# Kernel tuning notes

Measured on AMD Instinct MI355X. Metric: run time of the kernel, lower is better.

## Reference

```python
import jax, jax.numpy as jnp
import numpy as np

N_NODES = 50000
N_EDGES = 1600000
IN_FEATS = 128
ENC_H = 20
DEC_H = 64


def setup_inputs() -> dict:
    key = jax.random.key(0)
    ks = jax.random.split(key, 14)
    inp = {}
    inp["x"] = jax.random.normal(ks[0], (N_NODES, IN_FEATS), dtype=jnp.float32)
    inp["edge_index"] = jax.random.randint(ks[1], (2, N_EDGES), 0, N_NODES, dtype=jnp.int64)
    inp["node_id"] = 0
    inp["noise_normal"] = jax.random.normal(ks[2], (N_EDGES, ENC_H), dtype=jnp.float32)
    inp["noise_u"] = jax.random.uniform(ks[3], (N_EDGES, 1), dtype=jnp.float32)
    # parameters (glorot-ish init)
    def lin(k, fan_in, fan_out):
        s = 1.0 / np.sqrt(fan_in)
        return jax.random.uniform(k, (fan_in, fan_out), jnp.float32, -s, s)
    inp["W_gc"] = lin(ks[4], IN_FEATS, ENC_H)
    inp["b_gc"] = jnp.zeros((ENC_H,), jnp.float32)
    inp["W_mu"] = lin(ks[5], 3 * ENC_H, ENC_H)
    inp["b_mu"] = jnp.zeros((ENC_H,), jnp.float32)
    inp["W_var"] = lin(ks[6], 3 * ENC_H, ENC_H)
    inp["b_var"] = jnp.zeros((ENC_H,), jnp.float32)
    inp["W_d1"] = lin(ks[7], ENC_H, DEC_H)
    inp["b_d1"] = jnp.zeros((DEC_H,), jnp.float32)
    inp["W_d2"] = lin(ks[8], DEC_H, 1)
    inp["b_d2"] = jnp.zeros((1,), jnp.float32)
    return inp


def _gcn_conv(x, edge_index, W, b):
    """PyG-style GCNConv: add self-loops, symmetric D^-1/2 (A+I) D^-1/2 norm."""
    n = x.shape[0]
    sl = jnp.arange(n, dtype=edge_index.dtype)
    row = jnp.concatenate([edge_index[0], sl])  # source
    col = jnp.concatenate([edge_index[1], sl])  # target
    xw = x @ W  # [N, H]
    deg = jax.ops.segment_sum(jnp.ones_like(col, dtype=xw.dtype), col, num_segments=n)
    dinv = jnp.where(deg > 0, jax.lax.rsqrt(deg), 0.0)
    norm = dinv[row] * dinv[col]  # [E+N]
    out = jax.ops.segment_sum(xw[row] * norm[:, None], col, num_segments=n)
    return out + b


def reference(x, edge_index, node_id, noise_normal, noise_u,
              W_gc, b_gc, W_mu, b_mu, W_var, b_var, W_d1, b_d1, W_d2, b_d2):
    # GCN encoder
    x1 = jax.nn.relu(_gcn_conv(x, edge_index, W_gc, b_gc))  # [N, H]
    # per-edge concat: [src_embed | dst_embed | node_id_embed]
    rows, cols = edge_index[0], edge_index[1]
    node_embed = jnp.broadcast_to(x1[node_id][None, :], (rows.shape[0], x1.shape[1]))
    x2 = jnp.concatenate([x1[rows], x1[cols], node_embed], axis=1)  # [E, 3H]
    # variational heads + reparameterization
    mu = x2 @ W_mu + b_mu
    sigma = jnp.exp(x2 @ W_var + b_var)
    z = mu + sigma * noise_normal  # [E, H]
    # decoder MLP
    h = jax.nn.relu(z @ W_d1 + b_d1)
    sampling_weights = jax.nn.relu(h @ W_d2 + b_d2)  # [E, 1]
    # gumbel-sigmoid sample (training=True, bias=0.0 -> bias'=1e-4, temperature=1.0)
    bias = 0.0001
    eps = (bias - (1.0 - bias)) * noise_u + (1.0 - bias)
    gate = jnp.log(eps) - jnp.log(1.0 - eps) + sampling_weights
    return jax.nn.sigmoid(gate)
```

## Files before the change

### kernel.cpp

```cpp
#include <hip/hip_runtime.h>

#define NFEAT 128
#define H 20
#define DH 64
#define SCAN_T 1024
#define BE 64
#define NB 192
#define HW 12800

typedef __attribute__((ext_vector_type(8))) short short8;
typedef __attribute__((ext_vector_type(4))) float f32x4;

__device__ __forceinline__ unsigned short f2bf(float f) {
    union { float f; unsigned u; } v; v.f = f;
    unsigned r = v.u + 0x7fff + ((v.u >> 16) & 1);
    return (unsigned short)(r >> 16);
}
__device__ __forceinline__ unsigned pk2(unsigned short a, unsigned short b) {
    return (unsigned)a | ((unsigned)b << 16);
}

template <int CTRL>
__device__ __forceinline__ float dpp_add(float x) {
    int y = __builtin_amdgcn_update_dpp(0, __float_as_int(x), CTRL, 0xF, 0xF, true);
    return x + __int_as_float(y);
}
__device__ __forceinline__ float sum16(float x) {
    x = dpp_add<0xB1>(x);
    x = dpp_add<0x4E>(x);
    x = dpp_add<0x124>(x);
    x = dpp_add<0x128>(x);
    return x;
}

__global__ __launch_bounds__(256) void k_prep(const float* __restrict__ Wmu, const float* __restrict__ Wvar,
                                              const float* __restrict__ Wd1,
                                              unsigned short* __restrict__ Bh, unsigned short* __restrict__ Bd1,
                                              int* __restrict__ deg, int* __restrict__ csum, int N) {
    int t = blockIdx.x * blockDim.x + threadIdx.x;
    if (t < N) deg[t] = 0;
    if (t < 256) csum[t] = 0;
    if (t < 512) {
        int f = t >> 6, l = t & 63;
        int tile = f >> 1, s = f & 1;
        int col = (tile & 1) * 16 + (l & 15);
        const float* W = (tile < 2) ? Wmu : Wvar;
#pragma unroll
        for (int j = 0; j < 8; j++) {
            int k = s * 32 + (l >> 4) * 8 + j;
            float v = (k < 2 * H && col < H) ? W[k * H + col] : 0.f;
            Bh[(size_t)f * 512 + l * 8 + j] = f2bf(v);
        }
    } else if (t < 768) {
        int f = (t - 512) >> 6, l = t & 63;
        int n = f * 16 + (l & 15);
#pragma unroll
        for (int j = 0; j < 8; j++) {
            int k = (l >> 4) * 8 + j;
            float v = (k < H) ? Wd1[k * DH + n] : 0.f;
            Bd1[(size_t)f * 512 + l * 8 + j] = f2bf(v);
        }
    }
}

__global__ __launch_bounds__(512) void k_hist(const int* __restrict__ cols,
                                              unsigned* __restrict__ hist, int* __restrict__ csum,
                                              int E, int N) {
    __shared__ unsigned h[HW];
    __shared__ int cs[256];
    int wstride = (N + 3) >> 2;
    int nchunks = (N + 255) >> 8;
    for (int i = threadIdx.x; i < wstride; i += 512) h[i] = 0;
    if (threadIdx.x < 256) cs[threadIdx.x] = 0;
    __syncthreads();
    int chunk = (E + NB - 1) / NB;
    int beg = blockIdx.x * chunk, end = min(beg + chunk, E);
    for (int i = beg + threadIdx.x; i < end; i += 512) {
        int c = __builtin_nontemporal_load(cols + i);
        atomicAdd(&h[c >> 2], 1u << ((c & 3) * 8));
    }
    __syncthreads();
    unsigned* dst = hist + (size_t)blockIdx.x * wstride;
    for (int i = threadIdx.x; i < wstride; i += 512) {
        unsigned w = h[i];
        dst[i] = w;
        if (w) {
            int s = (w & 0xFF) + ((w >> 8) & 0xFF) + ((w >> 16) & 0xFF) + (w >> 24);
            atomicAdd(&cs[i >> 6], s);
        }
    }
    __syncthreads();
    for (int j = threadIdx.x; j < nchunks; j += 512)
        if (cs[j]) atomicAdd(&csum[j], cs[j]);
}

__global__ __launch_bounds__(256) void k_scansmall(const int* __restrict__ chunkSum,
                                                   int* __restrict__ chunkOff, int nb) {
    __shared__ int sc[256];
    int t = threadIdx.x;
    int v0 = (t < nb) ? chunkSum[t] : 0;
    sc[t] = v0;
    __syncthreads();
    for (int off = 1; off < 256; off <<= 1) {
        int v = (t >= off) ? sc[t - off] : 0;
        __syncthreads();
        sc[t] += v;
        __syncthreads();
    }
    if (t < nb) chunkOff[t] = sc[t] - v0;
}

__global__ __launch_bounds__(256) void k_bases(const unsigned* __restrict__ hist,
                                               const int* __restrict__ chunkOff,
                                               unsigned char* __restrict__ delta,
                                               int* __restrict__ offsets, int* __restrict__ deg,
                                               int N, int E) {
    __shared__ int sc[256];
    int c = blockIdx.x * 256 + threadIdx.x;
    int wstride = (N + 3) >> 2;
    int sh = (c & 3) * 8;
    bool valid = c < N;
    int cw = valid ? (c >> 2) : 0;
    unsigned cnt[NB / 4];
    int d = 0;
#pragma unroll
    for (int b = 0; b < NB; b++) {
        unsigned w = hist[(size_t)b * wstride + cw];
        unsigned byte = (w >> sh) & 0xFF;
        if ((b & 3) == 0) cnt[b >> 2] = byte;
        else cnt[b >> 2] |= byte << ((b & 3) * 8);
        d += (int)byte;
    }
    if (!valid) d = 0;
    sc[threadIdx.x] = d;
    __syncthreads();
    for (int off = 1; off < 256; off <<= 1) {
        int v = (threadIdx.x >= off) ? sc[threadIdx.x - off] : 0;
        __syncthreads();
        sc[threadIdx.x] += v;
        __syncthreads();
    }
    if (valid) {
        int base = chunkOff[blockIdx.x] + sc[threadIdx.x] - d;
        offsets[c] = base;
        deg[c] = d;
        int run = 0;
#pragma unroll
        for (int b = 0; b < NB; b++) {
            delta[(size_t)b * N + c] = (unsigned char)run;
            run += (int)((cnt[b >> 2] >> ((b & 3) * 8)) & 0xFF);
        }
    }
    if (blockIdx.x == 0 && threadIdx.x == 0) offsets[N] = E;
}

__global__ __launch_bounds__(512) void k_place(const int* __restrict__ rows, const int* __restrict__ cols,
                                               const int* __restrict__ offsets,
                                               const unsigned char* __restrict__ delta,
                                               unsigned short* __restrict__ srcs, int E, int N) {
    __shared__ unsigned h[HW];
    int wstride = (N + 3) >> 2;
    for (int i = threadIdx.x; i < wstride; i += 512) h[i] = 0;
    __syncthreads();
    int chunk = (E + NB - 1) / NB;
    int beg = blockIdx.x * chunk, end = min(beg + chunk, E);
    const unsigned char* mydelta = delta + (size_t)blockIdx.x * N;
    for (int i = beg + threadIdx.x; i < end; i += 512) {
        int c = __builtin_nontemporal_load(cols + i);
        int r = __builtin_nontemporal_load(rows + i);
        int sh = (c & 3) * 8;
        unsigned old = atomicAdd(&h[c >> 2], 1u << sh);
        int rank = (old >> sh) & 0xFF;
        int pos = offsets[c] + (int)mydelta[c] + rank;
        srcs[pos] = (unsigned short)r;
    }
}

__global__ __launch_bounds__(256) void k_deg(const int* __restrict__ cols, int* __restrict__ deg, int E) {
    int t = blockIdx.x * blockDim.x + threadIdx.x;
    if (t < E) atomicAdd(&deg[cols[t]], 1);
}

__global__ __launch_bounds__(SCAN_T) void k_scan(const int* __restrict__ deg, int* __restrict__ offsets,
                                                 int* __restrict__ cursor, int N) {
    __shared__ int sums[SCAN_T];
    int t = threadIdx.x;
    int chunk = (N + SCAN_T - 1) / SCAN_T;
    int beg = t * chunk;
    int end = min(beg + chunk, N);
    int s = 0;
    for (int i = beg; i < end; i++) s += deg[i];
    sums[t] = s;
    __syncthreads();
    for (int off = 1; off < SCAN_T; off <<= 1) {
        int v = (t >= off) ? sums[t - off] : 0;
        __syncthreads();
        sums[t] += v;
        __syncthreads();
    }
    int run = (t == 0) ? 0 : sums[t - 1];
    for (int i = beg; i < end; i++) {
        offsets[i] = run;
        cursor[i] = run;
        run += deg[i];
    }
    if (t == SCAN_T - 1) offsets[N] = sums[SCAN_T - 1];
}

__global__ __launch_bounds__(256) void k_bucket_csr(const int* __restrict__ rows, const int* __restrict__ cols,
                                                    int* __restrict__ cursor, int* __restrict__ srcs, int E) {
    int e = blockIdx.x * blockDim.x + threadIdx.x;
    if (e >= E) return;
    int pos = atomicAdd(&cursor[cols[e]], 1);
    srcs[pos] = rows[e];
}

__global__ __launch_bounds__(256) void k_xw_xs(const float* __restrict__ x, const float* __restrict__ Wgc,
                                               const int* __restrict__ deg,
                                               float* __restrict__ xs, int N) {
    __shared__ float Ws[NFEAT * H];
    for (int i = threadIdx.x; i < NFEAT * H; i += blockDim.x) Ws[i] = Wgc[i];
    __syncthreads();
    int n = blockIdx.x * blockDim.x + threadIdx.x;
    if (n >= N) return;
    float acc[H];
#pragma unroll
    for (int j = 0; j < H; j++) acc[j] = 0.f;
    const float4* x4 = (const float4*)(x + (size_t)n * NFEAT);
#pragma unroll 4
    for (int k4 = 0; k4 < NFEAT / 4; k4++) {
        float4 xv = x4[k4];
#pragma unroll
        for (int s = 0; s < 4; s++) {
            float xk = (s == 0) ? xv.x : (s == 1) ? xv.y : (s == 2) ? xv.z : xv.w;
            const float4* wrow = (const float4*)(Ws + (k4 * 4 + s) * H);
#pragma unroll
            for (int q = 0; q < 5; q++) {
                float4 w = wrow[q];
                acc[q * 4 + 0] += xk * w.x;
                acc[q * 4 + 1] += xk * w.y;
                acc[q * 4 + 2] += xk * w.z;
                acc[q * 4 + 3] += xk * w.w;
            }
        }
    }
    float di = rsqrtf((float)(deg[n] + 1));
    float4* o = (float4*)(xs + (size_t)n * H);
#pragma unroll
    for (int q = 0; q < 5; q++)
        o[q] = make_float4(acc[q * 4 + 0] * di, acc[q * 4 + 1] * di, acc[q * 4 + 2] * di, acc[q * 4 + 3] * di);
}

template <typename IT>
__device__ __forceinline__ void gather_core16(const float* __restrict__ xs, const IT* __restrict__ idx,
                                              int beg, int end, int n, int sl, int degn,
                                              const float* __restrict__ bgc, unsigned short* __restrict__ x1b,
                                              int nid, const float* __restrict__ Wmu, const float* __restrict__ Wvar,
                                              const float* __restrict__ bmu, const float* __restrict__ bvar,
                                              float* __restrict__ bcat2) {
    float acc[H];
    if (sl == 0) {
        const float4* self = (const float4*)(xs + (size_t)n * H);
#pragma unroll
        for (int q = 0; q < 5; q++) {
            float4 v = self[q];
            acc[q * 4 + 0] = v.x; acc[q * 4 + 1] = v.y; acc[q * 4 + 2] = v.z; acc[q * 4 + 3] = v.w;
        }
    } else {
#pragma unroll
        for (int j = 0; j < H; j++) acc[j] = 0.f;
    }
#pragma unroll 2
    for (int i = beg + sl; i < end; i += 16) {
        int r = (int)__builtin_nontemporal_load(idx + i);
        const float4* p = (const float4*)(xs + (size_t)r * H);
#pragma unroll
        for (int q = 0; q < 5; q++) {
            float4 v = p[q];
            acc[q * 4 + 0] += v.x; acc[q * 4 + 1] += v.y; acc[q * 4 + 2] += v.z; acc[q * 4 + 3] += v.w;
        }
    }
#pragma unroll
    for (int j = 0; j < H; j++) acc[j] = sum16(acc[j]);
    float di = rsqrtf((float)(degn + 1));
    float x1f[H];
#pragma unroll
    for (int j = 0; j < H; j++) x1f[j] = fmaxf(di * acc[j] + bgc[j], 0.f);
    if (sl == 0) {
        unsigned o[10];
#pragma unroll
        for (int j = 0; j < 10; j++) o[j] = pk2(f2bf(x1f[2 * j]), f2bf(x1f[2 * j + 1]));
        unsigned* dst = (unsigned*)(x1b + (size_t)n * H);
        *(uint4*)dst = make_uint4(o[0], o[1], o[2], o[3]);
        *(uint4*)(dst + 4) = make_uint4(o[4], o[5], o[6], o[7]);
        *(uint2*)(dst + 8) = make_uint2(o[8], o[9]);
    }
    if (n == nid) {
#pragma unroll
        for (int base = 0; base < 48; base += 16) {
            int jj = base + sl;
            if (jj < 40) {
                bool ismu = jj < 20;
                int col = ismu ? jj : jj - 20;
                const float* W = ismu ? Wmu : Wvar;
                float s = ismu ? bmu[col] : bvar[col];
#pragma unroll
                for (int k = 0; k < H; k++) s += x1f[k] * W[(2 * H + k) * H + col];
                bcat2[jj] = s;
            }
        }
    }
}

__global__ __launch_bounds__(256) void k_gather_csr16(const float* __restrict__ xs, const unsigned short* __restrict__ srcs,
                                                      const int* __restrict__ offsets, const int* __restrict__ deg,
                                                      const float* __restrict__ bgc,
                                                      unsigned short* __restrict__ x1b,
                                                      const int* __restrict__ node_id,
                                                      const float* __restrict__ Wmu, const float* __restrict__ Wvar,
                                                      const float* __restrict__ bmu, const float* __restrict__ bvar,
                                                      float* __restrict__ bcat2, int N) {
    int wave = (blockIdx.x * 256 + threadIdx.x) >> 6;
    int lane = threadIdx.x & 63;
    int n = wave * 4 + (lane >> 4);
    if (n >= N) return;
    gather_core16(xs, srcs, offsets[n], offsets[n + 1], n, lane & 15, deg[n], bgc, x1b,
                  node_id[0], Wmu, Wvar, bmu, bvar, bcat2);
}

__global__ __launch_bounds__(256) void k_gather_csr(const float* __restrict__ xs, const int* __restrict__ srcs,
                                                    const int* __restrict__ offsets, const int* __restrict__ deg,
                                                    const float* __restrict__ bgc,
                                                    unsigned short* __restrict__ x1b,
                                                    const int* __restrict__ node_id,
                                                    const float* __restrict__ Wmu, const float* __restrict__ Wvar,
                                                    const float* __restrict__ bmu, const float* __restrict__ bvar,
                                                    float* __restrict__ bcat2, int N) {
    int wave = (blockIdx.x * 256 + threadIdx.x) >> 6;
    int lane = threadIdx.x & 63;
    int n = wave * 4 + (lane >> 4);
    if (n >= N) return;
    gather_core16(xs, srcs, offsets[n], offsets[n + 1], n, lane & 15, deg[n], bgc, x1b,
                  node_id[0], Wmu, Wvar, bmu, bvar, bcat2);
}

__global__ __launch_bounds__(256, 8) void k_mlp(
    const unsigned short* __restrict__ x1b, const int* __restrict__ rows, const int* __restrict__ cols,
    const float* __restrict__ noise_n, const float* __restrict__ noise_u,
    const unsigned short* __restrict__ Bh, const unsigned short* __restrict__ Bd1g,
    const float* __restrict__ bcat2, const float* __restrict__ b_d1,
    const float* __restrict__ W_d2, const float* __restrict__ b_d2,
    float* __restrict__ out, int E) {

    __shared__ __align__(16) unsigned short x2s[BE * 72];
    __shared__ __align__(16) unsigned short A2[BE * 44];

    int tid = threadIdx.x;
    int e0 = blockIdx.x * BE;
    int l = tid & 63, w = tid >> 6;
    int m = l & 15, quad = l >> 4;
    int erow0 = w * 16 + quad * 4;

    float nz0[4], nz1[4];
#pragma unroll
    for (int r4 = 0; r4 < 4; r4++) {
        int e = e0 + erow0 + r4;
        int ec = (e < E) ? e : 0;
        nz0[r4] = noise_n[(size_t)ec * H + m];
        nz1[r4] = (m < 4) ? noise_n[(size_t)ec * H + 16 + m] : 0.f;
    }

    {
        int le = tid >> 2, p = tid & 3;
        int e = e0 + le; if (e >= E) e = E - 1;
        int r = rows[e], c = cols[e];
#pragma unroll
        for (int ii = 0; ii < 4; ii++) {
            int i = p + ii * 4;
            unsigned* dst = (unsigned*)((char*)x2s + le * 144 + i * 8);
            if (i < 10) {
                int node = (i < 5) ? r : c;
                int cc = (i < 5) ? i : i - 5;
                uint2 v = *(const uint2*)((const char*)x1b + (size_t)node * 40 + cc * 8);
                dst[0] = v.x;
                dst[1] = v.y;
            } else {
                dst[0] = 0u; dst[1] = 0u;
            }
        }
    }
    __syncthreads();

    f32x4 accs[4];
    {
        const char* arow = (const char*)x2s + (w * 16 + m) * 144 + quad * 16;
        short8 a0 = *(const short8*)(arow);
        short8 a1 = *(const short8*)(arow + 64);
#pragma unroll
        for (int t4 = 0; t4 < 4; t4++) {
            f32x4 acc = {0.f, 0.f, 0.f, 0.f};
            short8 b0 = *(const short8*)(Bh + (t4 * 2 + 0) * 512 + l * 8);
            short8 b1 = *(const short8*)(Bh + (t4 * 2 + 1) * 512 + l * 8);
            acc = __builtin_amdgcn_mfma_f32_16x16x32_bf16(a0, b0, acc, 0, 0, 0);
            acc = __builtin_amdgcn_mfma_f32_16x16x32_bf16(a1, b1, acc, 0, 0, 0);
            accs[t4] = acc;
        }
    }

    {
        float bm0 = bcat2[m];
        float bv0 = bcat2[20 + m];
        float bm1 = (m < 4) ? bcat2[16 + m] : 0.f;
        float bv1 = (m < 4) ? bcat2[36 + m] : 0.f;
#pragma unroll
        for (int r4 = 0; r4 < 4; r4++) {
            float z0 = accs[0][r4] + bm0 + __expf(accs[2][r4] + bv0) * nz0[r4];
            *(unsigned short*)((char*)A2 + (erow0 + r4) * 88 + m * 2) = f2bf(z0);
            unsigned short z1v = 0;
            if (m < 4) z1v = f2bf(accs[1][r4] + bm1 + __expf(accs[3][r4] + bv1) * nz1[r4]);
            *(unsigned short*)((char*)A2 + (erow0 + r4) * 88 + (16 + m) * 2) = z1v;
        }
    }
    __syncthreads();

    {
        short8 a2 = *(const short8*)((const char*)A2 + (w * 16 + m) * 88 + quad * 16);
        float p0 = 0.f, p1 = 0.f, p2 = 0.f, p3 = 0.f;
#pragma unroll
        for (int t4 = 0; t4 < 4; t4++) {
            f32x4 acc = {0.f, 0.f, 0.f, 0.f};
            short8 bb = *(const short8*)(Bd1g + t4 * 512 + l * 8);
            acc = __builtin_amdgcn_mfma_f32_16x16x32_bf16(a2, bb, acc, 0, 0, 0);
            int col = t4 * 16 + m;
            float bias = b_d1[col], wo = W_d2[col];
            p0 += fmaxf(acc[0] + bias, 0.f) * wo;
            p1 += fmaxf(acc[1] + bias, 0.f) * wo;
            p2 += fmaxf(acc[2] + bias, 0.f) * wo;
            p3 += fmaxf(acc[3] + bias, 0.f) * wo;
        }
        p0 = sum16(p0); p1 = sum16(p1); p2 = sum16(p2); p3 = sum16(p3);
        if (m < 4) {
            float swv = (m == 0) ? p0 : (m == 1) ? p1 : (m == 2) ? p2 : p3;
            int leo = w * 16 + quad * 4 + m;
            int e = e0 + leo;
            if (e < E) {
                float sw = fmaxf(swv + b_d2[0], 0.f);
                float u = noise_u[e];
                float ev = 0.9999f - 0.9998f * u;
                float t = __expf(-sw);
                out[e] = ev / (ev + (1.f - ev) * t);
            }
        }
    }
}

extern "C" void kernel_launch(void* const* d_in, const int* in_sizes, int n_in,
                              void* d_out, int out_size, void* d_ws, size_t ws_size,
                              hipStream_t stream) {
    const int N = in_sizes[0] / NFEAT;
    const int E = in_sizes[1] / 2;

    const float* x       = (const float*)d_in[0];
    const int*   ei      = (const int*)d_in[1];
    const int*   rows    = ei;
    const int*   cols    = ei + E;
    const int*   node_id = (const int*)d_in[2];
    const float* noise_n = (const float*)d_in[3];
    const float* noise_u = (const float*)d_in[4];
    const float* Wgc  = (const float*)d_in[5];
    const float* bgc  = (const float*)d_in[6];
    const float* Wmu  = (const float*)d_in[7];
    const float* bmu  = (const float*)d_in[8];
    const float* Wvar = (const float*)d_in[9];
    const float* bvar = (const float*)d_in[10];
    const float* Wd1  = (const float*)d_in[11];
    const float* bd1  = (const float*)d_in[12];
    const float* Wd2  = (const float*)d_in[13];
    const float* bd2  = (const float*)d_in[14];
    float* out = (float*)d_out;

    const int B = 256;
    int gN  = (N + B - 1) / B;
    int gG  = (N + 15) / 16;
    int gE  = (E + B - 1) / B;
    int gM  = (E + BE - 1) / BE;
    int nBins = (N + 255) / 256;

    char* ws = (char*)d_ws;
    size_t o_deg     = 0;
    size_t o_off     = o_deg  + (((size_t)N * 4 + 255) & ~255ULL);
    size_t o_csum    = o_off  + (((size_t)(N + 1) * 4 + 255) & ~255ULL);
    size_t o_coff    = o_csum + 1024;
    size_t o_hist    = o_coff + 1024;
    size_t wstride   = (size_t)((N + 3) >> 2);
    size_t o_delta   = o_hist  + ((NB * wstride * 4 + 255) & ~255ULL);
    size_t o_srcs    = o_delta + (((size_t)NB * N + 255) & ~255ULL);
    size_t o_xs      = o_srcs  + (((size_t)E * 2 + 255) & ~255ULL);
    size_t o_x1b     = o_xs    + (((size_t)N * H * 4 + 255) & ~255ULL);
    size_t o_Bh      = o_x1b   + (((size_t)N * H * 2 + 255) & ~255ULL);
    size_t o_Bd1     = o_Bh    + 8192;
    size_t o_bcat2   = o_Bd1   + 4096;
    size_t need      = o_bcat2 + 256;

    bool main_path = (ws_size >= need) && (N <= 4 * HW) && (N < 65536) && (nBins <= 256);

    if (main_path) {
        int*   deg     = (int*)(ws + o_deg);
        int*   offsets = (int*)(ws + o_off);
        int*   csum    = (int*)(ws + o_csum);
        int*   coff    = (int*)(ws + o_coff);
        unsigned* hist = (unsigned*)(ws + o_hist);
        unsigned char* delta = (unsigned char*)(ws + o_delta);
        unsigned short* srcs = (unsigned short*)(ws + o_srcs);
        float* xs      = (float*)(ws + o_xs);
        unsigned short* x1b  = (unsigned short*)(ws + o_x1b);
        unsigned short* Bh   = (unsigned short*)(ws + o_Bh);
        unsigned short* Bd1  = (unsigned short*)(ws + o_Bd1);
        float* bcat2   = (float*)(ws + o_bcat2);

        k_prep<<<gN, B, 0, stream>>>(Wmu, Wvar, Wd1, Bh, Bd1, deg, csum, N);
        k_hist<<<NB, 512, 0, stream>>>(cols, hist, csum, E, N);
        k_scansmall<<<1, B, 0, stream>>>(csum, coff, nBins);
        k_bases<<<nBins, B, 0, stream>>>(hist, coff, delta, offsets, deg, N, E);
        k_xw_xs<<<gN, B, 0, stream>>>(x, Wgc, deg, xs, N);
        k_place<<<NB, 512, 0, stream>>>(rows, cols, offsets, delta, srcs, E, N);
        k_gather_csr16<<<gG, B, 0, stream>>>(xs, srcs, offsets, deg, bgc, x1b,
                                             node_id, Wmu, Wvar, bmu, bvar, bcat2, N);
        k_mlp<<<gM, B, 0, stream>>>(x1b, rows, cols, noise_n, noise_u,
                                    Bh, Bd1, bcat2, bd1, Wd2, bd2, out, E);
    } else {
        int*   deg     = (int*)ws;
        int*   offsets = (int*)(ws + 200000);
        int*   cursor  = (int*)(ws + 400016);
        int*   srcs    = (int*)(ws + 600016);
        float* xs      = (float*)(ws + 7000016);
        unsigned short* x1b = (unsigned short*)(ws + 11000016);
        unsigned short* Bh  = (unsigned short*)(ws + 13000016);
        unsigned short* Bd1 = (unsigned short*)(ws + 13008208);
        float* bcat2   = (float*)(ws + 13012304);

        k_prep<<<gN, B, 0, stream>>>(Wmu, Wvar, Wd1, Bh, Bd1, deg, cursor, N);
        k_deg<<<gE, B, 0, stream>>>(cols, deg, E);
        k_scan<<<1, SCAN_T, 0, stream>>>(deg, offsets, cursor, N);
        k_bucket_csr<<<gE, B, 0, stream>>>(rows, cols, cursor, srcs, E);
        k_xw_xs<<<gN, B, 0, stream>>>(x, Wgc, deg, xs, N);
        k_gather_csr<<<gG, B, 0, stream>>>(xs, srcs, offsets, deg, bgc, x1b,
                                           node_id, Wmu, Wvar, bmu, bvar, bcat2, N);
        k_mlp<<<gM, B, 0, stream>>>(x1b, rows, cols, noise_n, noise_u,
                                    Bh, Bd1, bcat2, bd1, Wd2, bd2, out, E);
    }
}
```

Before: 430.4 us.

## Record per-edge rank in histogram pass and drop LDS from edge MLP

The histogram kernel now saves each edge's within-block rank from its shared-memory atomic into a byte array. The placement kernel therefore becomes a simple per-edge scatter with no shared histogram rebuild. The edge MLP kernel is restructured to compute the transposed product: each lane loads its edge's embeddings straight from global memory as the MFMA operand, and the intermediate z is shuffled with ds_bpermute instead of two LDS round-trips and barriers. This adds an E-byte rank buffer and extra writes, and changes the bcat2 layout, which is now zero-initialised in prep.

```diff
diff --git a/kernel.cpp b/kernel.cpp
--- a/kernel.cpp
+++ b/kernel.cpp
@@ -35,21 +35,23 @@
 
 __global__ __launch_bounds__(256) void k_prep(const float* __restrict__ Wmu, const float* __restrict__ Wvar,
                                               const float* __restrict__ Wd1,
-                                              unsigned short* __restrict__ Bh, unsigned short* __restrict__ Bd1,
-                                              int* __restrict__ deg, int* __restrict__ csum, int N) {
+                                              unsigned short* __restrict__ Bh2, unsigned short* __restrict__ Bd1,
+                                              int* __restrict__ deg, int* __restrict__ csum,
+                                              float* __restrict__ bcat2, int N) {
     int t = blockIdx.x * blockDim.x + threadIdx.x;
     if (t < N) deg[t] = 0;
     if (t < 256) csum[t] = 0;
+    if (t < 128) bcat2[t] = 0.f;
     if (t < 512) {
         int f = t >> 6, l = t & 63;
-        int tile = f >> 1, s = f & 1;
-        int col = (tile & 1) * 16 + (l & 15);
-        const float* W = (tile < 2) ? Wmu : Wvar;
+        int h = f >> 2, tt = (f >> 1) & 1, s = f & 1;
+        const float* W = h ? Wvar : Wmu;
+        int d = tt * 16 + (l & 15);
 #pragma unroll
         for (int j = 0; j < 8; j++) {
             int k = s * 32 + (l >> 4) * 8 + j;
-            float v = (k < 2 * H && col < H) ? W[k * H + col] : 0.f;
-            Bh[(size_t)f * 512 + l * 8 + j] = f2bf(v);
+            float v = (k < 2 * H && d < H) ? W[k * H + d] : 0.f;
+            Bh2[(size_t)f * 512 + l * 8 + j] = f2bf(v);
         }
     } else if (t < 768) {
         int f = (t - 512) >> 6, l = t & 63;
@@ -65,6 +67,7 @@
 
 __global__ __launch_bounds__(512) void k_hist(const int* __restrict__ cols,
                                               unsigned* __restrict__ hist, int* __restrict__ csum,
+                                              unsigned char* __restrict__ rank,
                                               int E, int N) {
     __shared__ unsigned h[HW];
     __shared__ int cs[256];
@@ -77,7 +80,9 @@
     int beg = blockIdx.x * chunk, end = min(beg + chunk, E);
     for (int i = beg + threadIdx.x; i < end; i += 512) {
         int c = __builtin_nontemporal_load(cols + i);
-        atomicAdd(&h[c >> 2], 1u << ((c & 3) * 8));
+        int sh = (c & 3) * 8;
+        unsigned old = atomicAdd(&h[c >> 2], 1u << sh);
+        rank[i] = (unsigned char)((old >> sh) & 0xFF);
     }
     __syncthreads();
     unsigned* dst = hist + (size_t)blockIdx.x * wstride;
@@ -154,26 +159,18 @@
     if (blockIdx.x == 0 && threadIdx.x == 0) offsets[N] = E;
 }
 
-__global__ __launch_bounds__(512) void k_place(const int* __restrict__ rows, const int* __restrict__ cols,
+__global__ __launch_bounds__(256) void k_place(const int* __restrict__ rows, const int* __restrict__ cols,
                                                const int* __restrict__ offsets,
                                                const unsigned char* __restrict__ delta,
-                                               unsigned short* __restrict__ srcs, int E, int N) {
-    __shared__ unsigned h[HW];
-    int wstride = (N + 3) >> 2;
-    for (int i = threadIdx.x; i < wstride; i += 512) h[i] = 0;
-    __syncthreads();
-    int chunk = (E + NB - 1) / NB;
-    int beg = blockIdx.x * chunk, end = min(beg + chunk, E);
-    const unsigned char* mydelta = delta + (size_t)blockIdx.x * N;
-    for (int i = beg + threadIdx.x; i < end; i += 512) {
-        int c = __builtin_nontemporal_load(cols + i);
-        int r = __builtin_nontemporal_load(rows + i);
-        int sh = (c & 3) * 8;
-        unsigned old = atomicAdd(&h[c >> 2], 1u << sh);
-        int rank = (old >> sh) & 0xFF;
-        int pos = offsets[c] + (int)mydelta[c] + rank;
-        srcs[pos] = (unsigned short)r;
-    }
+                                               const unsigned char* __restrict__ rank,
+                                               unsigned short* __restrict__ srcs, int E, int N, int chunk) {
+    int e = blockIdx.x * 256 + threadIdx.x;
+    if (e >= E) return;
+    int c = cols[e];
+    int r = rows[e];
+    int b = e / chunk;
+    int pos = offsets[c] + (int)delta[(size_t)b * N + c] + (int)rank[e];
+    srcs[pos] = (unsigned short)r;
 }
 
 __global__ __launch_bounds__(256) void k_deg(const int* __restrict__ cols, int* __restrict__ deg, int E) {
@@ -306,7 +303,7 @@
                 float s = ismu ? bmu[col] : bvar[col];
 #pragma unroll
                 for (int k = 0; k < H; k++) s += x1f[k] * W[(2 * H + k) * H + col];
-                bcat2[jj] = s;
+                bcat2[ismu ? col : 64 + col] = s;
             }
         }
     }
@@ -344,112 +341,123 @@
                   node_id[0], Wmu, Wvar, bmu, bvar, bcat2);
 }
 
-__global__ __launch_bounds__(256, 8) void k_mlp(
+__global__ __launch_bounds__(256) void k_mlp(
     const unsigned short* __restrict__ x1b, const int* __restrict__ rows, const int* __restrict__ cols,
     const float* __restrict__ noise_n, const float* __restrict__ noise_u,
-    const unsigned short* __restrict__ Bh, const unsigned short* __restrict__ Bd1g,
+    const unsigned short* __restrict__ Bh2, const unsigned short* __restrict__ Bd1g,
     const float* __restrict__ bcat2, const float* __restrict__ b_d1,
     const float* __restrict__ W_d2, const float* __restrict__ b_d2,
     float* __restrict__ out, int E) {
 
-    __shared__ __align__(16) unsigned short x2s[BE * 72];
-    __shared__ __align__(16) unsigned short A2[BE * 44];
-
     int tid = threadIdx.x;
     int e0 = blockIdx.x * BE;
     int l = tid & 63, w = tid >> 6;
-    int m = l & 15, quad = l >> 4;
-    int erow0 = w * 16 + quad * 4;
-
-    float nz0[4], nz1[4];
-#pragma unroll
-    for (int r4 = 0; r4 < 4; r4++) {
-        int e = e0 + erow0 + r4;
-        int ec = (e < E) ? e : 0;
-        nz0[r4] = noise_n[(size_t)ec * H + m];
-        nz1[r4] = (m < 4) ? noise_n[(size_t)ec * H + 16 + m] : 0.f;
-    }
-
-    {
-        int le = tid >> 2, p = tid & 3;
-        int e = e0 + le; if (e >= E) e = E - 1;
-        int r = rows[e], c = cols[e];
-#pragma unroll
-        for (int ii = 0; ii < 4; ii++) {
-            int i = p + ii * 4;
-            unsigned* dst = (unsigned*)((char*)x2s + le * 144 + i * 8);
-            if (i < 10) {
-                int node = (i < 5) ? r : c;
-                int cc = (i < 5) ? i : i - 5;
-                uint2 v = *(const uint2*)((const char*)x1b + (size_t)node * 40 + cc * 8);
-                dst[0] = v.x;
-                dst[1] = v.y;
-            } else {
-                dst[0] = 0u; dst[1] = 0u;
-            }
-        }
-    }
-    __syncthreads();
+    int m = l & 15, g = l >> 4;
+
+    int ea = e0 + w * 16 + m;
+    int em = (ea < E) ? ea : E - 1;
+    int r = rows[em], c = cols[em];
+
+    const char* br = (const char*)x1b + (size_t)r * 40;
+    const char* bc = (const char*)x1b + (size_t)c * 40;
+    const char* a0p = (g == 0) ? br : (g == 1) ? br + 16 : (g == 2) ? br + 32 : bc + 8;
+    const char* a1p = (g == 0) ? br + 8 : (g == 1) ? br + 24 : (g == 2) ? bc : bc + 16;
+    uint2 f0a = *(const uint2*)a0p;
+    uint2 f0b = *(const uint2*)a1p;
+    union U8 { unsigned u[4]; short8 s; };
+    U8 B0u, B1u;
+    B0u.u[0] = f0a.x; B0u.u[1] = f0a.y; B0u.u[2] = f0b.x; B0u.u[3] = f0b.y;
+    B1u.u[0] = 0u; B1u.u[1] = 0u; B1u.u[2] = 0u; B1u.u[3] = 0u;
+    if (g == 0) {
+        uint2 f1a = *(const uint2*)(bc + 24);
+        uint2 f1b = *(const uint2*)(bc + 32);
+        B1u.u[0] = f1a.x; B1u.u[1] = f1a.y; B1u.u[2] = f1b.x; B1u.u[3] = f1b.y;
+    }
+
+    float4 nz0 = *(const float4*)(noise_n + (size_t)em * H + g * 4);
+    float4 bm0 = *(const float4*)(bcat2 + g * 4);
+    float4 bv0 = *(const float4*)(bcat2 + 64 + g * 4);
+    float4 nz1 = make_float4(0.f, 0.f, 0.f, 0.f), bm1 = nz1, bv1 = nz1;
+    if (g == 0) {
+        nz1 = *(const float4*)(noise_n + (size_t)em * H + 16);
+        bm1 = *(const float4*)(bcat2 + 16);
+        bv1 = *(const float4*)(bcat2 + 80);
+    }
 
     f32x4 accs[4];
-    {
-        const char* arow = (const char*)x2s + (w * 16 + m) * 144 + quad * 16;
-        short8 a0 = *(const short8*)(arow);
-        short8 a1 = *(const short8*)(arow + 64);
-#pragma unroll
-        for (int t4 = 0; t4 < 4; t4++) {
-            f32x4 acc = {0.f, 0.f, 0.f, 0.f};
-            short8 b0 = *(const short8*)(Bh + (t4 * 2 + 0) * 512 + l * 8);
-            short8 b1 = *(const short8*)(Bh + (t4 * 2 + 1) * 512 + l * 8);
-            acc = __builtin_amdgcn_mfma_f32_16x16x32_bf16(a0, b0, acc, 0, 0, 0);
-            acc = __builtin_amdgcn_mfma_f32_16x16x32_bf16(a1, b1, acc, 0, 0, 0);
-            accs[t4] = acc;
-        }
-    }
-
-    {
-        float bm0 = bcat2[m];
-        float bv0 = bcat2[20 + m];
-        float bm1 = (m < 4) ? bcat2[16 + m] : 0.f;
-        float bv1 = (m < 4) ? bcat2[36 + m] : 0.f;
-#pragma unroll
-        for (int r4 = 0; r4 < 4; r4++) {
-            float z0 = accs[0][r4] + bm0 + __expf(accs[2][r4] + bv0) * nz0[r4];
-            *(unsigned short*)((char*)A2 + (erow0 + r4) * 88 + m * 2) = f2bf(z0);
-            unsigned short z1v = 0;
-            if (m < 4) z1v = f2bf(accs[1][r4] + bm1 + __expf(accs[3][r4] + bv1) * nz1[r4]);
-            *(unsigned short*)((char*)A2 + (erow0 + r4) * 88 + (16 + m) * 2) = z1v;
-        }
-    }
-    __syncthreads();
-
-    {
-        short8 a2 = *(const short8*)((const char*)A2 + (w * 16 + m) * 88 + quad * 16);
-        float p0 = 0.f, p1 = 0.f, p2 = 0.f, p3 = 0.f;
-#pragma unroll
-        for (int t4 = 0; t4 < 4; t4++) {
-            f32x4 acc = {0.f, 0.f, 0.f, 0.f};
-            short8 bb = *(const short8*)(Bd1g + t4 * 512 + l * 8);
-            acc = __builtin_amdgcn_mfma_f32_16x16x32_bf16(a2, bb, acc, 0, 0, 0);
-            int col = t4 * 16 + m;
-            float bias = b_d1[col], wo = W_d2[col];
-            p0 += fmaxf(acc[0] + bias, 0.f) * wo;
-            p1 += fmaxf(acc[1] + bias, 0.f) * wo;
-            p2 += fmaxf(acc[2] + bias, 0.f) * wo;
-            p3 += fmaxf(acc[3] + bias, 0.f) * wo;
-        }
-        p0 = sum16(p0); p1 = sum16(p1); p2 = sum16(p2); p3 = sum16(p3);
-        if (m < 4) {
-            float swv = (m == 0) ? p0 : (m == 1) ? p1 : (m == 2) ? p2 : p3;
-            int leo = w * 16 + quad * 4 + m;
-            int e = e0 + leo;
-            if (e < E) {
-                float sw = fmaxf(swv + b_d2[0], 0.f);
-                float u = noise_u[e];
-                float ev = 0.9999f - 0.9998f * u;
-                float t = __expf(-sw);
-                out[e] = ev / (ev + (1.f - ev) * t);
-            }
+#pragma unroll
+    for (int q4 = 0; q4 < 4; q4++) {
+        f32x4 acc = {0.f, 0.f, 0.f, 0.f};
+        short8 A0 = *(const short8*)(Bh2 + (q4 * 2 + 0) * 512 + l * 8);
+        short8 A1 = *(const short8*)(Bh2 + (q4 * 2 + 1) * 512 + l * 8);
+        acc = __builtin_amdgcn_mfma_f32_16x16x32_bf16(A0, B0u.s, acc, 0, 0, 0);
+        acc = __builtin_amdgcn_mfma_f32_16x16x32_bf16(A1, B1u.s, acc, 0, 0, 0);
+        accs[q4] = acc;
+    }
+
+    float nza[4] = {nz0.x, nz0.y, nz0.z, nz0.w};
+    float bma[4] = {bm0.x, bm0.y, bm0.z, bm0.w};
+    float bva[4] = {bv0.x, bv0.y, bv0.z, bv0.w};
+    float nzb[4] = {nz1.x, nz1.y, nz1.z, nz1.w};
+    float bmb[4] = {bm1.x, bm1.y, bm1.z, bm1.w};
+    float bvb[4] = {bv1.x, bv1.y, bv1.z, bv1.w};
+    float z0[4], z1[4];
+#pragma unroll
+    for (int rr = 0; rr < 4; rr++) {
+        z0[rr] = accs[0][rr] + bma[rr] + __expf(accs[2][rr] + bva[rr]) * nza[rr];
+        z1[rr] = 0.f;
+    }
+    if (g == 0) {
+#pragma unroll
+        for (int rr = 0; rr < 4; rr++)
+            z1[rr] = accs[1][rr] + bmb[rr] + __expf(accs[3][rr] + bvb[rr]) * nzb[rr];
+    }
+    unsigned pz0 = pk2(f2bf(z0[0]), f2bf(z0[1]));
+    unsigned pz1 = pk2(f2bf(z0[2]), f2bf(z0[3]));
+    unsigned pz2 = pk2(f2bf(z1[0]), f2bf(z1[1]));
+    unsigned pz3 = pk2(f2bf(z1[2]), f2bf(z1[3]));
+
+    int sA = (((2 * g) & 3) * 16 + m) * 4;
+    int sB = (((2 * g + 1) & 3) * 16 + m) * 4;
+    unsigned qA0 = (unsigned)__builtin_amdgcn_ds_bpermute(sA, (int)pz0);
+    unsigned qA1 = (unsigned)__builtin_amdgcn_ds_bpermute(sA, (int)pz1);
+    unsigned qB0 = (unsigned)__builtin_amdgcn_ds_bpermute(sB, (int)pz0);
+    unsigned qB1 = (unsigned)__builtin_amdgcn_ds_bpermute(sB, (int)pz1);
+    unsigned qA2 = (unsigned)__builtin_amdgcn_ds_bpermute(sA, (int)pz2);
+    unsigned qA3 = (unsigned)__builtin_amdgcn_ds_bpermute(sA, (int)pz3);
+    unsigned qB2 = (unsigned)__builtin_amdgcn_ds_bpermute(sB, (int)pz2);
+    unsigned qB3 = (unsigned)__builtin_amdgcn_ds_bpermute(sB, (int)pz3);
+    bool hi = (g == 2);
+    U8 A2u;
+    A2u.u[0] = (g == 3) ? 0u : (hi ? qA2 : qA0);
+    A2u.u[1] = (g == 3) ? 0u : (hi ? qA3 : qA1);
+    A2u.u[2] = (g == 3) ? 0u : (hi ? qB2 : qB0);
+    A2u.u[3] = (g == 3) ? 0u : (hi ? qB3 : qB1);
+    short8 a2 = A2u.s;
+
+    float p0 = 0.f, p1 = 0.f, p2 = 0.f, p3 = 0.f;
+#pragma unroll
+    for (int t4 = 0; t4 < 4; t4++) {
+        f32x4 acc = {0.f, 0.f, 0.f, 0.f};
+        short8 bb = *(const short8*)(Bd1g + t4 * 512 + l * 8);
+        acc = __builtin_amdgcn_mfma_f32_16x16x32_bf16(a2, bb, acc, 0, 0, 0);
+        int col = t4 * 16 + m;
+        float bias = b_d1[col], wo = W_d2[col];
+        p0 += fmaxf(acc[0] + bias, 0.f) * wo;
+        p1 += fmaxf(acc[1] + bias, 0.f) * wo;
+        p2 += fmaxf(acc[2] + bias, 0.f) * wo;
+        p3 += fmaxf(acc[3] + bias, 0.f) * wo;
+    }
+    p0 = sum16(p0); p1 = sum16(p1); p2 = sum16(p2); p3 = sum16(p3);
+    if (m < 4) {
+        float swv = (m == 0) ? p0 : (m == 1) ? p1 : (m == 2) ? p2 : p3;
+        int e = e0 + w * 16 + g * 4 + m;
+        if (e < E) {
+            float sw = fmaxf(swv + b_d2[0], 0.f);
+            float u = noise_u[e];
+            float ev = 0.9999f - 0.9998f * u;
+            float t = __expf(-sw);
+            out[e] = ev / (ev + (1.f - ev) * t);
         }
     }
 }
@@ -485,22 +493,24 @@
     int gE  = (E + B - 1) / B;
     int gM  = (E + BE - 1) / BE;
     int nBins = (N + 255) / 256;
+    int chunk = (E + NB - 1) / NB;
 
     char* ws = (char*)d_ws;
+    size_t wstride   = (size_t)((N + 3) >> 2);
     size_t o_deg     = 0;
     size_t o_off     = o_deg  + (((size_t)N * 4 + 255) & ~255ULL);
     size_t o_csum    = o_off  + (((size_t)(N + 1) * 4 + 255) & ~255ULL);
     size_t o_coff    = o_csum + 1024;
     size_t o_hist    = o_coff + 1024;
-    size_t wstride   = (size_t)((N + 3) >> 2);
     size_t o_delta   = o_hist  + ((NB * wstride * 4 + 255) & ~255ULL);
-    size_t o_srcs    = o_delta + (((size_t)NB * N + 255) & ~255ULL);
+    size_t o_rank    = o_delta + (((size_t)NB * N + 255) & ~255ULL);
+    size_t o_srcs    = o_rank  + (((size_t)E + 255) & ~255ULL);
     size_t o_xs      = o_srcs  + (((size_t)E * 2 + 255) & ~255ULL);
     size_t o_x1b     = o_xs    + (((size_t)N * H * 4 + 255) & ~255ULL);
-    size_t o_Bh      = o_x1b   + (((size_t)N * H * 2 + 255) & ~255ULL);
-    size_t o_Bd1     = o_Bh    + 8192;
+    size_t o_Bh2     = o_x1b   + (((size_t)N * H * 2 + 255) & ~255ULL);
+    size_t o_Bd1     = o_Bh2   + 8192;
     size_t o_bcat2   = o_Bd1   + 4096;
-    size_t need      = o_bcat2 + 256;
+    size_t need      = o_bcat2 + 512;
 
     bool main_path = (ws_size >= need) && (N <= 4 * HW) && (N < 65536) && (nBins <= 256);
 
@@ -511,35 +521,46 @@
         int*   coff    = (int*)(ws + o_coff);
         unsigned* hist = (unsigned*)(ws + o_hist);
         unsigned char* delta = (unsigned char*)(ws + o_delta);
+        unsigned char* rank  = (unsigned char*)(ws + o_rank);
         unsigned short* srcs = (unsigned short*)(ws + o_srcs);
         float* xs      = (float*)(ws + o_xs);
         unsigned short* x1b  = (unsigned short*)(ws + o_x1b);
-        unsigned short* Bh   = (unsigned short*)(ws + o_Bh);
+        unsigned short* Bh2  = (unsigned short*)(ws + o_Bh2);
         unsigned short* Bd1  = (unsigned short*)(ws + o_Bd1);
         float* bcat2   = (float*)(ws + o_bcat2);
 
-        k_prep<<<gN, B, 0, stream>>>(Wmu, Wvar, Wd1, Bh, Bd1, deg, csum, N);
-        k_hist<<<NB, 512, 0, stream>>>(cols, hist, csum, E, N);
+        k_prep<<<gN, B, 0, stream>>>(Wmu, Wvar, Wd1, Bh2, Bd1, deg, csum, bcat2, N);
+        k_hist<<<NB, 512, 0, stream>>>(cols, hist, csum, rank, E, N);
         k_scansmall<<<1, B, 0, stream>>>(csum, coff, nBins);
         k_bases<<<nBins, B, 0, stream>>>(hist, coff, delta, offsets, deg, N, E);
         k_xw_xs<<<gN, B, 0, stream>>>(x, Wgc, deg, xs, N);
-        k_place<<<NB, 512, 0, stream>>>(rows, cols, offsets, delta, srcs, E, N);
+        k_place<<<gE, B, 0, stream>>>(rows, cols, offsets, delta, rank, srcs, E, N, chunk);
         k_gather_csr16<<<gG, B, 0, stream>>>(xs, srcs, offsets, deg, bgc, x1b,
                                              node_id, Wmu, Wvar, bmu, bvar, bcat2, N);
         k_mlp<<<gM, B, 0, stream>>>(x1b, rows, cols, noise_n, noise_u,
-                                    Bh, Bd1, bcat2, bd1, Wd2, bd2, out, E);
+                                    Bh2, Bd1, bcat2, bd1, Wd2, bd2, out, E);
     } else {
-        int*   deg     = (int*)ws;
-        int*   offsets = (int*)(ws + 200000);
-        int*   cursor  = (int*)(ws + 400016);
-        int*   srcs    = (int*)(ws + 600016);
-        float* xs      = (float*)(ws + 7000016);
-        unsigned short* x1b = (unsigned short*)(ws + 11000016);
-        unsigned short* Bh  = (unsigned short*)(ws + 13000016);
-        unsigned short* Bd1 = (unsigned short*)(ws + 13008208);
-        float* bcat2   = (float*)(ws + 13012304);
-
-        k_prep<<<gN, B, 0, stream>>>(Wmu, Wvar, Wd1, Bh, Bd1, deg, cursor, N);
+        size_t f_deg   = 0;
+        size_t f_off   = f_deg + (((size_t)N * 4 + 255) & ~255ULL);
+        size_t f_cur   = f_off + (((size_t)(N + 1) * 4 + 255) & ~255ULL);
+        size_t f_srcs  = f_cur + (((size_t)N * 4 + 255) & ~255ULL);
+        size_t f_xs    = f_srcs + (((size_t)E * 4 + 255) & ~255ULL);
+        size_t f_x1b   = f_xs + (((size_t)N * H * 4 + 255) & ~255ULL);
+        size_t f_Bh2   = f_x1b + (((size_t)N * H * 2 + 255) & ~255ULL);
+        size_t f_Bd1   = f_Bh2 + 8192;
+        size_t f_bcat2 = f_Bd1 + 4096;
+
+        int*   deg     = (int*)(ws + f_deg);
+        int*   offsets = (int*)(ws + f_off);
+        int*   cursor  = (int*)(ws + f_cur);
+        int*   srcs    = (int*)(ws + f_srcs);
+        float* xs      = (float*)(ws + f_xs);
+        unsigned short* x1b = (unsigned short*)(ws + f_x1b);
+        unsigned short* Bh2 = (unsigned short*)(ws + f_Bh2);
+        unsigned short* Bd1 = (unsigned short*)(ws + f_Bd1);
+        float* bcat2   = (float*)(ws + f_bcat2);
+
+        k_prep<<<gN, B, 0, stream>>>(Wmu, Wvar, Wd1, Bh2, Bd1, deg, cursor, bcat2, N);
         k_deg<<<gE, B, 0, stream>>>(cols, deg, E);
         k_scan<<<1, SCAN_T, 0, stream>>>(deg, offsets, cursor, N);
         k_bucket_csr<<<gE, B, 0, stream>>>(rows, cols, cursor, srcs, E);
@@ -547,6 +568,6 @@
         k_gather_csr<<<gG, B, 0, stream>>>(xs, srcs, offsets, deg, bgc, x1b,
                                            node_id, Wmu, Wvar, bmu, bvar, bcat2, N);
         k_mlp<<<gM, B, 0, stream>>>(x1b, rows, cols, noise_n, noise_u,
-                                    Bh, Bd1, bcat2, bd1, Wd2, bd2, out, E);
-    }
-}
+                                    Bh2, Bd1, bcat2, bd1, Wd2, bd2, out, E);
+    }
+}
```

Result: no change. 428.4 us (-0.5%).
